# Optimization experiments

Measured on AMD Instinct MI355X. Metric: run time of the kernel, lower is better.

Reference implementation:

```python
import jax, jax.numpy as jnp
import numpy as np
from jax import lax


def _conv(x, w, b):
    # x: [B,C,H,W] NCHW, w: [O,I,3,3] OIHW, SAME padding, stride 1
    y = lax.conv_general_dilated(x, w, (1, 1), 'SAME',
                                 dimension_numbers=('NCHW', 'OIHW', 'NCHW'))
    return y + b[None, :, None, None]


def _maxpool2(x):
    return lax.reduce_window(x, -jnp.inf, lax.max,
                             (1, 1, 2, 2), (1, 1, 2, 2), 'VALID')


def _squash(x):
    # x: [..., D]
    norm = jnp.sum(x * x, axis=-1, keepdims=True)
    scale = norm / (1.0 + norm) / jnp.sqrt(norm + 1e-9)
    return scale * x


def _routing(x, W):
    # x: [B, R, C]  (R routes, C in_channels); W: [N, R, C, O]
    # u_hat[b,n,r,o] = sum_c x[b,r,c] * W[n,r,c,o]
    u_hat = jnp.einsum('brc,nrco->bnro', x, W)
    B, N, R, O = u_hat.shape
    b_ij = jnp.zeros((B, N, R), dtype=u_hat.dtype)
    v = None
    for it in range(3):  # fixed 3 routing iterations
        c_ij = jax.nn.softmax(b_ij, axis=2)
        s_j = jnp.einsum('bnr,bnro->bno', c_ij, u_hat)
        v = _squash(s_j)
        if it < 2:
            b_ij = b_ij + jnp.einsum('bnro,bno->bnr', u_hat, v)
    return v  # [B, N, O]


def setup_inputs() -> dict:
    key = jax.random.key(0)
    ks = jax.random.split(key, 10)
    B = 512
    num_classes = 15
    x = jax.random.normal(ks[0], (B, 3, 64, 64), dtype=jnp.float32)

    def kaiming(k, shape, fan_in):
        return jax.random.normal(k, shape, dtype=jnp.float32) * np.sqrt(2.0 / fan_in)

    w1 = kaiming(ks[1], (8, 3, 3, 3), 3 * 9)
    b1 = jnp.zeros((8,), jnp.float32)
    w2 = kaiming(ks[2], (16, 8, 3, 3), 8 * 9)
    b2 = jnp.zeros((16,), jnp.float32)
    w3 = kaiming(ks[3], (32, 16, 3, 3), 16 * 9)
    b3 = jnp.zeros((32,), jnp.float32)
    # route_weights are torch.randn in the original (std 1.0)
    rw1 = jax.random.normal(ks[4], (32, 64, 32, 8), dtype=jnp.float32)   # primary
    rw2 = jax.random.normal(ks[5], (num_classes, 32, 8, 16), dtype=jnp.float32)  # secondary
    fc_w = kaiming(ks[6], (num_classes, 16 * num_classes), 16 * num_classes)
    fc_b = jnp.zeros((num_classes,), jnp.float32)
    return {'x': x, 'w1': w1, 'b1': b1, 'w2': w2, 'b2': b2,
            'w3': w3, 'b3': b3, 'rw1': rw1, 'rw2': rw2,
            'fc_w': fc_w, 'fc_b': fc_b}


def reference(x, w1, b1, w2, b2, w3, b3, rw1, rw2, fc_w, fc_b):
    h = _maxpool2(jax.nn.relu(_conv(x, w1, b1)))   # [B,8,32,32]
    h = _maxpool2(jax.nn.relu(_conv(h, w2, b2)))   # [B,16,16,16]
    h = _maxpool2(jax.nn.relu(_conv(h, w3, b3)))   # [B,32,8,8]
    B = h.shape[0]
    # routes = 64 spatial positions, channels = 32 capsule input features
    feats = h.reshape(B, 32, 64).transpose(0, 2, 1)  # [B, 64, 32]
    v1 = _routing(feats, rw1)   # [B, 32, 8]
    v2 = _routing(v1, rw2)      # [B, 15, 16]
    flat = v2.reshape(B, -1)    # [B, 240]
    return flat @ fc_w.T + fc_b  # [B, 15]
```

## Files before the change

kernel.cpp:

```cpp
#include <hip/hip_runtime.h>
#include <hip/hip_bf16.h>


template<int CIN, int COUT, int HIN, int NO>
__global__ __launch_bounds__(256)
void conv_relu_pool(const float* __restrict__ in, const float* __restrict__ w,
                    const float* __restrict__ bias, float* __restrict__ out)
{
    constexpr int HOUT = HIN / 2;
    constexpr int PR = HIN + 2;
    constexpr int PC = (HIN + 2 + 3) & ~3;
    constexpr int NS = HIN / 8;
    constexpr int NOP = COUT / NO;
    constexpr int NTASK = NOP * HOUT * NS;
    constexpr int XWORDS = CIN * PR * PC;
    constexpr int WWORDS = CIN * 9 * COUT;

    __shared__ float xin[CIN][PR][PC];
    __shared__ float wt[WWORDS];
    __shared__ float bl[COUT];

    const int tid = threadIdx.x;
    const int b   = blockIdx.x;

    for (int i = tid; i < XWORDS; i += 256) ((float*)xin)[i] = 0.f;
    for (int i = tid; i < WWORDS; i += 256) {
        int o = i % COUT, k = (i / COUT) % 9, c = i / (COUT * 9);
        wt[i] = w[(o * CIN + c) * 9 + k];
    }
    if (tid < COUT) bl[tid] = bias[tid];
    __syncthreads();

    const float4* gin = (const float4*)(in + (size_t)b * CIN * HIN * HIN);
    constexpr int CHUNKS = CIN * HIN * (HIN / 4);
    for (int i = tid; i < CHUNKS; i += 256) {
        float4 v = gin[i];
        int ch = i % (HIN / 4);
        int y  = (i / (HIN / 4)) % HIN;
        int c  = i / ((HIN / 4) * HIN);
        float* dst = &xin[c][y + 1][ch * 4 + 1];
        dst[0] = v.x; dst[1] = v.y; dst[2] = v.z; dst[3] = v.w;
    }
    __syncthreads();

    for (int task = tid; task < NTASK; task += 256) {
        const int s  = task % NS;
        const int py = (task / NS) % HOUT;
        const int o0 = (task / (NS * HOUT)) * NO;
        const int X0 = s * 8;

        float acc[NO][2][8];
#pragma unroll
        for (int n = 0; n < NO; ++n)
#pragma unroll
            for (int q = 0; q < 2; ++q)
#pragma unroll
                for (int j = 0; j < 8; ++j) acc[n][q][j] = 0.f;

        for (int c = 0; c < CIN; ++c) {
            float rows[4][12];
#pragma unroll
            for (int rr = 0; rr < 4; ++rr) {
                const float4* src = (const float4*)&xin[c][2 * py + rr][X0];
#pragma unroll
                for (int j = 0; j < 3; ++j) {
                    float4 v = src[j];
                    rows[rr][j * 4 + 0] = v.x; rows[rr][j * 4 + 1] = v.y;
                    rows[rr][j * 4 + 2] = v.z; rows[rr][j * 4 + 3] = v.w;
                }
            }
            const float* wc = wt + c * 9 * COUT;
#pragma unroll
            for (int ky = 0; ky < 3; ++ky) {
#pragma unroll
                for (int n = 0; n < NO; ++n) {
                    const float w0 = wc[(ky * 3 + 0) * COUT + o0 + n];
                    const float w1 = wc[(ky * 3 + 1) * COUT + o0 + n];
                    const float w2 = wc[(ky * 3 + 2) * COUT + o0 + n];
#pragma unroll
                    for (int j = 0; j < 8; ++j) {
                        acc[n][0][j] = fmaf(rows[ky][j],     w0, acc[n][0][j]);
                        acc[n][0][j] = fmaf(rows[ky][j + 1], w1, acc[n][0][j]);
                        acc[n][0][j] = fmaf(rows[ky][j + 2], w2, acc[n][0][j]);
                        acc[n][1][j] = fmaf(rows[ky + 1][j],     w0, acc[n][1][j]);
                        acc[n][1][j] = fmaf(rows[ky + 1][j + 1], w1, acc[n][1][j]);
                        acc[n][1][j] = fmaf(rows[ky + 1][j + 2], w2, acc[n][1][j]);
                    }
                }
            }
        }
#pragma unroll
        for (int n = 0; n < NO; ++n) {
            const float bv = bl[o0 + n];
            float4 ov;
            float* p = (float*)&ov;
#pragma unroll
            for (int j = 0; j < 4; ++j) {
                float m = fmaxf(fmaxf(acc[n][0][2 * j], acc[n][0][2 * j + 1]),
                                fmaxf(acc[n][1][2 * j], acc[n][1][2 * j + 1]));
                p[j] = fmaxf(m + bv, 0.f);
            }
            float* po = out + (((size_t)b * COUT + o0 + n) * HOUT + py) * HOUT + s * 4;
            *(float4*)po = ov;
        }
    }
}

__global__ __launch_bounds__(256)
void transpose_w1(const float* __restrict__ W, float* __restrict__ Wt)
{
    int idx = blockIdx.x * 256 + threadIdx.x;
    if (idx >= 32 * 32 * 64 * 2) return;
    int half = idx & 1;
    int r    = (idx >> 1) & 63;
    int c    = (idx >> 7) & 31;
    int n    = idx >> 12;
    ((float4*)Wt)[idx] =
        ((const float4*)W)[(((n * 64 + r) * 32 + c) << 1) + half];
}

__global__ __launch_bounds__(256)
void routing1_reg(const float* __restrict__ h3, const float* __restrict__ Wt,
                  float* __restrict__ v1)
{
    constexpr int C = 32, R = 64, O = 8, G = 4;
    const int lane = threadIdx.x & 63;
    const int n    = blockIdx.y * 4 + (threadIdx.x >> 6);
    const int b0   = blockIdx.x * G;

    float u[G][O];
#pragma unroll
    for (int g = 0; g < G; ++g)
#pragma unroll
        for (int o = 0; o < O; ++o) u[g][o] = 0.f;

    const float4* wp = (const float4*)Wt + (size_t)n * C * R * 2;
    const float* xb = h3 + (size_t)b0 * (C * R) + lane;

#pragma unroll 4
    for (int c = 0; c < C; ++c) {
        float xv[G];
#pragma unroll
        for (int g = 0; g < G; ++g) xv[g] = xb[(size_t)g * (C * R) + c * R];
        float4 w0 = wp[(c * R + lane) * 2];
        float4 w1 = wp[(c * R + lane) * 2 + 1];
#pragma unroll
        for (int g = 0; g < G; ++g) {
            u[g][0] = fmaf(xv[g], w0.x, u[g][0]);
            u[g][1] = fmaf(xv[g], w0.y, u[g][1]);
            u[g][2] = fmaf(xv[g], w0.z, u[g][2]);
            u[g][3] = fmaf(xv[g], w0.w, u[g][3]);
            u[g][4] = fmaf(xv[g], w1.x, u[g][4]);
            u[g][5] = fmaf(xv[g], w1.y, u[g][5]);
            u[g][6] = fmaf(xv[g], w1.z, u[g][6]);
            u[g][7] = fmaf(xv[g], w1.w, u[g][7]);
        }
    }

    float bij[G];
#pragma unroll
    for (int g = 0; g < G; ++g) bij[g] = 0.f;
    float v[G][O];

    for (int it = 0; it < 3; ++it) {
        float cc[G];
#pragma unroll
        for (int g = 0; g < G; ++g) {
            float mx = bij[g];
#pragma unroll
            for (int w = 1; w < 64; w <<= 1) mx = fmaxf(mx, __shfl_xor(mx, w, 64));
            float e = __expf(bij[g] - mx);
            float sum = e;
#pragma unroll
            for (int w = 1; w < 64; w <<= 1) sum += __shfl_xor(sum, w, 64);
            cc[g] = e / sum;
        }
        float s[G][O];
#pragma unroll
        for (int g = 0; g < G; ++g)
#pragma unroll
            for (int o = 0; o < O; ++o) s[g][o] = cc[g] * u[g][o];
#pragma unroll
        for (int w = 1; w < 64; w <<= 1)
#pragma unroll
            for (int g = 0; g < G; ++g)
#pragma unroll
                for (int o = 0; o < O; ++o) s[g][o] += __shfl_xor(s[g][o], w, 64);
#pragma unroll
        for (int g = 0; g < G; ++g) {
            float nr = 0.f;
#pragma unroll
            for (int o = 0; o < O; ++o) nr = fmaf(s[g][o], s[g][o], nr);
            float scale = nr / (1.f + nr) / sqrtf(nr + 1e-9f);
#pragma unroll
            for (int o = 0; o < O; ++o) v[g][o] = scale * s[g][o];
        }
        if (it < 2) {
#pragma unroll
            for (int g = 0; g < G; ++g) {
                float d = 0.f;
#pragma unroll
                for (int o = 0; o < O; ++o) d = fmaf(u[g][o], v[g][o], d);
                bij[g] += d;
            }
        }
    }
    if (lane < G * O) {
        int g = lane >> 3, o = lane & 7;
        v1[(size_t)(b0 + g) * 256 + n * 8 + o] = v[g][o];
    }
}

__global__ __launch_bounds__(256)
void routing2_fc(const float* __restrict__ v1, const float* __restrict__ W,
                 const float* __restrict__ fcw, const float* __restrict__ fcb,
                 float* __restrict__ out)
{
    constexpr int N = 15, R = 32, C = 8, O = 16;
    __shared__ float u[N * R * O];
    __shared__ float xl[R * C];
    __shared__ float bij[N * R];
    __shared__ float cij[N * R];
    __shared__ float vv[N * O];

    int t = threadIdx.x;
    int b = blockIdx.x;

    for (int i = t; i < R * C; i += 256) xl[i] = v1[(size_t)b * (R * C) + i];
    for (int i = t; i < N * R; i += 256) bij[i] = 0.f;
    __syncthreads();

    for (int i = t; i < N * R * O; i += 256) {
        int o = i % O;
        int r = (i / O) % R;
        int n = i / (O * R);
        const float* wp = W + ((size_t)(n * R + r) * C) * O + o;
        const float* xp = xl + r * C;
        float s = 0.f;
#pragma unroll
        for (int c = 0; c < C; ++c) s = fmaf(xp[c], wp[c * O], s);
        u[i] = s;
    }
    __syncthreads();

    for (int it = 0; it < 3; ++it) {
        if (t < 240) {
            int n = t >> 4, j = t & 15;
            float b0 = bij[n * R + j * 2], b1 = bij[n * R + j * 2 + 1];
            float mx = fmaxf(b0, b1);
            for (int w = 1; w < 16; w <<= 1) mx = fmaxf(mx, __shfl_xor(mx, w, 64));
            float e0 = __expf(b0 - mx), e1 = __expf(b1 - mx);
            float sum = e0 + e1;
            for (int w = 1; w < 16; w <<= 1) sum += __shfl_xor(sum, w, 64);
            float inv = 1.f / sum;
            cij[n * R + j * 2] = e0 * inv;
            cij[n * R + j * 2 + 1] = e1 * inv;
        }
        __syncthreads();
        if (t < 240) {
            int n = t >> 4, o = t & 15;
            float s = 0.f;
            for (int r = 0; r < R; ++r)
                s = fmaf(cij[n * R + r], u[(n * R + r) * O + o], s);
            float nr = s * s;
            for (int w = 1; w < 16; w <<= 1) nr += __shfl_xor(nr, w, 64);
            float scale = nr / (1.f + nr) / sqrtf(nr + 1e-9f);
            vv[t] = scale * s;
        }
        __syncthreads();
        if (it < 2) {
            for (int i = t; i < N * R; i += 256) {
                int n = i / R, r = i % R;
                const float* up = u + (n * R + r) * O;
                const float* vp = vv + n * O;
                float s = 0.f;
#pragma unroll
                for (int o = 0; o < O; ++o) s = fmaf(up[o], vp[o], s);
                bij[i] += s;
            }
            __syncthreads();
        }
    }
    if (t < 15) {
        float s = fcb[t];
        for (int k = 0; k < 240; ++k) s = fmaf(vv[k], fcw[t * 240 + k], s);
        out[(size_t)b * 15 + t] = s;
    }
}

extern "C" void kernel_launch(void* const* d_in, const int* in_sizes, int n_in,
                              void* d_out, int out_size, void* d_ws, size_t ws_size,
                              hipStream_t stream) {
    const float* x    = (const float*)d_in[0];
    const float* w1   = (const float*)d_in[1];
    const float* b1   = (const float*)d_in[2];
    const float* w2   = (const float*)d_in[3];
    const float* b2   = (const float*)d_in[4];
    const float* w3   = (const float*)d_in[5];
    const float* b3   = (const float*)d_in[6];
    const float* rw1  = (const float*)d_in[7];
    const float* rw2  = (const float*)d_in[8];
    const float* fcw  = (const float*)d_in[9];
    const float* fcb  = (const float*)d_in[10];
    float* out = (float*)d_out;

    const int B = 512;
    float* ws = (float*)d_ws;
    float* h1 = ws;
    float* h2 = h1 + (size_t)B * 8 * 32 * 32;
    float* h3 = h2 + (size_t)B * 16 * 16 * 16;
    float* v1 = h3 + (size_t)B * 32 * 8 * 8;
    float* Wt = h2;

    conv_relu_pool<3, 8, 64, 4><<<B, 256, 0, stream>>>(x, w1, b1, h1);
    conv_relu_pool<8, 16, 32, 4><<<B, 256, 0, stream>>>(h1, w2, b2, h2);
    conv_relu_pool<16, 32, 16, 2><<<B, 256, 0, stream>>>(h2, w3, b3, h3);
    transpose_w1<<<(32 * 32 * 64 * 2 + 255) / 256, 256, 0, stream>>>(rw1, Wt);
    {
        dim3 grid(B / 4, 8);
        routing1_reg<<<grid, 256, 0, stream>>>(h3, Wt, v1);
    }
    routing2_fc<<<B, 256, 0, stream>>>(v1, rw2, fcw, fcb, out);
}
```

Measured before the change: 226.4 us.

## Register-resident routing2 with wave-level reductions and parallel FC; batch 8 in routing1

Routing2 is rewritten so each wave holds u_hat for two output capsules in registers, with one lane per route, and runs softmax and the weighted sum through 32-lane shuffles. This replaces the shared-memory version that needed several __syncthreads per iteration. The final FC is spread over 240 threads with shuffle reductions instead of 15 serial threads. Routing1 now processes 8 batch items per block instead of 4, reusing each weight load across more samples at the cost of more registers and possible lower occupancy.

```diff
diff --git a/kernel.cpp b/kernel.cpp
--- a/kernel.cpp
+++ b/kernel.cpp
@@ -123,7 +123,7 @@
 void routing1_reg(const float* __restrict__ h3, const float* __restrict__ Wt,
                   float* __restrict__ v1)
 {
-    constexpr int C = 32, R = 64, O = 8, G = 4;
+    constexpr int C = 32, R = 64, O = 8, G = 8;
     const int lane = threadIdx.x & 63;
     const int n    = blockIdx.y * 4 + (threadIdx.x >> 6);
     const int b0   = blockIdx.x * G;
@@ -137,7 +137,7 @@
     const float4* wp = (const float4*)Wt + (size_t)n * C * R * 2;
     const float* xb = h3 + (size_t)b0 * (C * R) + lane;
 
-#pragma unroll 4
+#pragma unroll 2
     for (int c = 0; c < C; ++c) {
         float xv[G];
 #pragma unroll
@@ -160,7 +160,7 @@
     float bij[G];
 #pragma unroll
     for (int g = 0; g < G; ++g) bij[g] = 0.f;
-    float v[G][O];
+    float s[G][O];
 
     for (int it = 0; it < 3; ++it) {
         float cc[G];
@@ -175,7 +175,6 @@
             for (int w = 1; w < 64; w <<= 1) sum += __shfl_xor(sum, w, 64);
             cc[g] = e / sum;
         }
-        float s[G][O];
 #pragma unroll
         for (int g = 0; g < G; ++g)
 #pragma unroll
@@ -193,22 +192,22 @@
             for (int o = 0; o < O; ++o) nr = fmaf(s[g][o], s[g][o], nr);
             float scale = nr / (1.f + nr) / sqrtf(nr + 1e-9f);
 #pragma unroll
-            for (int o = 0; o < O; ++o) v[g][o] = scale * s[g][o];
-        }
-        if (it < 2) {
-#pragma unroll
-            for (int g = 0; g < G; ++g) {
+            for (int o = 0; o < O; ++o) s[g][o] *= scale;
+            if (it < 2) {
                 float d = 0.f;
 #pragma unroll
-                for (int o = 0; o < O; ++o) d = fmaf(u[g][o], v[g][o], d);
+                for (int o = 0; o < O; ++o) d = fmaf(u[g][o], s[g][o], d);
                 bij[g] += d;
             }
         }
     }
-    if (lane < G * O) {
-        int g = lane >> 3, o = lane & 7;
-        v1[(size_t)(b0 + g) * 256 + n * 8 + o] = v[g][o];
-    }
+    float outv = 0.f;
+#pragma unroll
+    for (int g = 0; g < G; ++g)
+#pragma unroll
+        for (int o = 0; o < O; ++o)
+            outv = (lane == g * O + o) ? s[g][o] : outv;
+    v1[(size_t)(b0 + (lane >> 3)) * 256 + n * 8 + (lane & 7)] = outv;
 }
 
 __global__ __launch_bounds__(256)
@@ -216,75 +215,96 @@
                  const float* __restrict__ fcw, const float* __restrict__ fcb,
                  float* __restrict__ out)
 {
-    constexpr int N = 15, R = 32, C = 8, O = 16;
-    __shared__ float u[N * R * O];
-    __shared__ float xl[R * C];
-    __shared__ float bij[N * R];
-    __shared__ float cij[N * R];
-    __shared__ float vv[N * O];
-
-    int t = threadIdx.x;
-    int b = blockIdx.x;
-
-    for (int i = t; i < R * C; i += 256) xl[i] = v1[(size_t)b * (R * C) + i];
-    for (int i = t; i < N * R; i += 256) bij[i] = 0.f;
+    constexpr int R = 32, C = 8, O = 16;
+    __shared__ float vv[240];
+
+    const int t  = threadIdx.x;
+    const int b  = blockIdx.x;
+    const int wv = t >> 6;
+    const int lane = t & 63;
+    const int nh = lane >> 5;
+    const int r  = lane & 31;
+
+    const float4* xr = (const float4*)(v1 + (size_t)b * 256 + r * 8);
+    float4 x0 = xr[0], x1 = xr[1];
+    float xv[8] = {x0.x, x0.y, x0.z, x0.w, x1.x, x1.y, x1.z, x1.w};
+
+    float u[2][O];
+    int nn[2];
+#pragma unroll
+    for (int p = 0; p < 2; ++p) {
+        int n = wv * 4 + p * 2 + nh;
+        nn[p] = n;
+        int ncl = n < 15 ? n : 14;
+        const float4* wp = (const float4*)(W + ((size_t)(ncl * R + r) * C) * O);
+#pragma unroll
+        for (int o = 0; o < O; ++o) u[p][o] = 0.f;
+#pragma unroll
+        for (int c = 0; c < C; ++c) {
+#pragma unroll
+            for (int j = 0; j < 4; ++j) {
+                float4 w4 = wp[c * 4 + j];
+                u[p][j * 4 + 0] = fmaf(xv[c], w4.x, u[p][j * 4 + 0]);
+                u[p][j * 4 + 1] = fmaf(xv[c], w4.y, u[p][j * 4 + 1]);
+                u[p][j * 4 + 2] = fmaf(xv[c], w4.z, u[p][j * 4 + 2]);
+                u[p][j * 4 + 3] = fmaf(xv[c], w4.w, u[p][j * 4 + 3]);
+            }
+        }
+    }
+
+    float bij[2] = {0.f, 0.f};
+    float s[2][O];
+    for (int it = 0; it < 3; ++it) {
+#pragma unroll
+        for (int p = 0; p < 2; ++p) {
+            float mx = bij[p];
+#pragma unroll
+            for (int w = 1; w < 32; w <<= 1) mx = fmaxf(mx, __shfl_xor(mx, w, 32));
+            float e = __expf(bij[p] - mx);
+            float sum = e;
+#pragma unroll
+            for (int w = 1; w < 32; w <<= 1) sum += __shfl_xor(sum, w, 32);
+            float cc = e / sum;
+#pragma unroll
+            for (int o = 0; o < O; ++o) s[p][o] = cc * u[p][o];
+        }
+#pragma unroll
+        for (int w = 1; w < 32; w <<= 1)
+#pragma unroll
+            for (int p = 0; p < 2; ++p)
+#pragma unroll
+                for (int o = 0; o < O; ++o) s[p][o] += __shfl_xor(s[p][o], w, 32);
+#pragma unroll
+        for (int p = 0; p < 2; ++p) {
+            float nr = 0.f;
+#pragma unroll
+            for (int o = 0; o < O; ++o) nr = fmaf(s[p][o], s[p][o], nr);
+            float scale = nr / (1.f + nr) / sqrtf(nr + 1e-9f);
+#pragma unroll
+            for (int o = 0; o < O; ++o) s[p][o] *= scale;
+            if (it < 2) {
+                float d = 0.f;
+#pragma unroll
+                for (int o = 0; o < O; ++o) d = fmaf(u[p][o], s[p][o], d);
+                bij[p] += d;
+            }
+        }
+    }
+#pragma unroll
+    for (int p = 0; p < 2; ++p) {
+        float outv = 0.f;
+#pragma unroll
+        for (int o = 0; o < O; ++o) outv = (r == o) ? s[p][o] : outv;
+        if (r < O && nn[p] < 15) vv[nn[p] * O + r] = outv;
+    }
     __syncthreads();
-
-    for (int i = t; i < N * R * O; i += 256) {
-        int o = i % O;
-        int r = (i / O) % R;
-        int n = i / (O * R);
-        const float* wp = W + ((size_t)(n * R + r) * C) * O + o;
-        const float* xp = xl + r * C;
-        float s = 0.f;
-#pragma unroll
-        for (int c = 0; c < C; ++c) s = fmaf(xp[c], wp[c * O], s);
-        u[i] = s;
-    }
-    __syncthreads();
-
-    for (int it = 0; it < 3; ++it) {
-        if (t < 240) {
-            int n = t >> 4, j = t & 15;
-            float b0 = bij[n * R + j * 2], b1 = bij[n * R + j * 2 + 1];
-            float mx = fmaxf(b0, b1);
-            for (int w = 1; w < 16; w <<= 1) mx = fmaxf(mx, __shfl_xor(mx, w, 64));
-            float e0 = __expf(b0 - mx), e1 = __expf(b1 - mx);
-            float sum = e0 + e1;
-            for (int w = 1; w < 16; w <<= 1) sum += __shfl_xor(sum, w, 64);
-            float inv = 1.f / sum;
-            cij[n * R + j * 2] = e0 * inv;
-            cij[n * R + j * 2 + 1] = e1 * inv;
-        }
-        __syncthreads();
-        if (t < 240) {
-            int n = t >> 4, o = t & 15;
-            float s = 0.f;
-            for (int r = 0; r < R; ++r)
-                s = fmaf(cij[n * R + r], u[(n * R + r) * O + o], s);
-            float nr = s * s;
-            for (int w = 1; w < 16; w <<= 1) nr += __shfl_xor(nr, w, 64);
-            float scale = nr / (1.f + nr) / sqrtf(nr + 1e-9f);
-            vv[t] = scale * s;
-        }
-        __syncthreads();
-        if (it < 2) {
-            for (int i = t; i < N * R; i += 256) {
-                int n = i / R, r = i % R;
-                const float* up = u + (n * R + r) * O;
-                const float* vp = vv + n * O;
-                float s = 0.f;
-#pragma unroll
-                for (int o = 0; o < O; ++o) s = fmaf(up[o], vp[o], s);
-                bij[i] += s;
-            }
-            __syncthreads();
-        }
-    }
-    if (t < 15) {
-        float s = fcb[t];
-        for (int k = 0; k < 240; ++k) s = fmaf(vv[k], fcw[t * 240 + k], s);
-        out[(size_t)b * 15 + t] = s;
+    if (t < 240) {
+        int j = t >> 4, k0 = t & 15;
+        float acc = 0.f;
+        for (int k = k0; k < 240; k += 16) acc = fmaf(vv[k], fcw[j * 240 + k], acc);
+#pragma unroll
+        for (int w = 1; w < 16; w <<= 1) acc += __shfl_xor(acc, w, 16);
+        if (k0 == 0) out[(size_t)b * 15 + j] = acc + fcb[j];
     }
 }
 
@@ -317,7 +337,7 @@
     conv_relu_pool<16, 32, 16, 2><<<B, 256, 0, stream>>>(h2, w3, b3, h3);
     transpose_w1<<<(32 * 32 * 64 * 2 + 255) / 256, 256, 0, stream>>>(rw1, Wt);
     {
-        dim3 grid(B / 4, 8);
+        dim3 grid(B / 8, 8);
         routing1_reg<<<grid, 256, 0, stream>>>(h3, Wt, v1);
     }
     routing2_fc<<<B, 256, 0, stream>>>(v1, rw2, fcw, fcb, out);
```

New measurement: 232.5 us. 1.03x slower.
